# Performance work log

Measured on AMD Instinct MI355X. Metric: run time of the kernel, lower is better.

## Reference

```python
import jax, jax.numpy as jnp
import numpy as np

M, K, N, GROUP = 64, 4096, 11008, 128
NGROUPS = K // GROUP  # 32


def setup_inputs() -> dict:
    key = jax.random.key(0)
    k1, k2, k3, k4, k5 = jax.random.split(key, 5)
    x = jax.random.normal(k1, (M, K), dtype=jnp.float32)
    # packed int4 weights: 8 nibbles per int32, full 32-bit entropy
    qweight = jax.random.bits(k2, (K // 8, N), dtype=jnp.uint32).astype(jnp.int32)
    qzeros = jax.random.bits(k3, (NGROUPS, N // 8), dtype=jnp.uint32).astype(jnp.int32)
    scales = jax.random.uniform(k4, (NGROUPS, N), dtype=jnp.float32, minval=0.001, maxval=0.02)
    bias = jax.random.normal(k5, (N,), dtype=jnp.float32) * 0.01
    return {"x": x, "qweight": qweight, "qzeros": qzeros, "scales": scales, "bias": bias}


def dequantize(qweight, qzeros, scales):
    shifts = jnp.arange(8, dtype=jnp.int32) * 4  # nibble bit offsets 0..28
    # unpack weights: [K//8, N] -> [K//8, 8, N] -> [NGROUPS, GROUP, N]
    w = (jnp.right_shift(qweight[:, None, :], shifts[None, :, None]) & 15)
    w = w.reshape(-1, GROUP, qweight.shape[1])
    # unpack zeros: [NGROUPS, N//8] -> [NGROUPS, N//8, 8] -> [NGROUPS, 1, N]; GPTQ stores zero-1
    z = (jnp.right_shift(qzeros[:, :, None], shifts[None, None, :]) & 15) + 1
    z = z.reshape(z.shape[0], 1, -1)
    # scale * (q - zero), per group: [NGROUPS, GROUP, N] -> [K, N]
    W = scales[:, None, :] * (w - z).astype(scales.dtype)
    return W.reshape(-1, W.shape[2])


def reference(x, qweight, qzeros, scales, bias):
    W = dequantize(qweight, qzeros, scales)  # [K, N] fp32
    return jnp.matmul(x, W.astype(x.dtype)) + bias
```

## Files before the change

kernel.cpp:

```cpp
#include <hip/hip_runtime.h>
#include <hip/hip_bf16.h>

namespace {

constexpr int MM = 64;
constexpr int KK = 4096;
constexpr int NN = 11008;
constexpr int NZROW = NN / 8;
constexpr int BN = 128;
constexpr int KSPLIT = 8;
constexpr int KSEG = KK / KSPLIT;
constexpr int NTILES = NN / BN;
constexpr int BK = 32;
constexpr int NCH = KSEG / BK;
constexpr int NG = 4;
constexpr size_t XB_OFF_BYTES = (size_t)KSPLIT * MM * NN * 4;
constexpr size_t WS_NEED = XB_OFF_BYTES + (size_t)MM * KK * 2;

typedef float f32x4 __attribute__((ext_vector_type(4)));
typedef short s16x8 __attribute__((ext_vector_type(8)));
typedef int   i32x4 __attribute__((ext_vector_type(4)));

__device__ __forceinline__ int pack_bf16(float a, float b) {
  union { __hip_bfloat162 h; int i; } u;
  u.h.x = __float2bfloat16(a);
  u.h.y = __float2bfloat16(b);
  return u.i;
}

__global__ __launch_bounds__(256) void xcvt_kernel(
    const float* __restrict__ x, unsigned short* __restrict__ xb)
{
  const int i8 = (blockIdx.x * 256 + threadIdx.x) * 8;
  const f32x4 a = *(const f32x4*)(x + i8);
  const f32x4 b = *(const f32x4*)(x + i8 + 4);
  i32x4 p;
  p.x = pack_bf16(a.x, a.y);
  p.y = pack_bf16(a.z, a.w);
  p.z = pack_bf16(b.x, b.y);
  p.w = pack_bf16(b.z, b.w);
  *(i32x4*)(xb + i8) = p;
}

__global__ __launch_bounds__(256) void prep_kernel(
    const float* __restrict__ bias, float* __restrict__ out)
{
  const int i = blockIdx.x * 256 + threadIdx.x;
  out[i] = bias[i % NN];
}

__global__ __launch_bounds__(256) void reduce_kernel(
    const float* __restrict__ ws, const float* __restrict__ bias,
    float* __restrict__ out)
{
  const int i4 = (blockIdx.x * 256 + threadIdx.x) * 4;
  f32x4 acc = *(const f32x4*)(bias + (i4 % NN));
  #pragma unroll
  for (int s = 0; s < KSPLIT; ++s)
    acc += *(const f32x4*)(ws + (size_t)s * (MM * NN) + i4);
  *(f32x4*)(out + i4) = acc;
}

template<bool WS>
__global__ __launch_bounds__(256, 4) void gptq_gemm_kernel(
    const float* __restrict__ x, const int* __restrict__ qw,
    const int* __restrict__ qz, const float* __restrict__ scales,
    const unsigned short* __restrict__ xb, float* __restrict__ out)
{
  const int tid  = threadIdx.x;
  const int wave = tid >> 6;
  const int lane = tid & 63;
  const int c    = lane & 15;
  const int quad = lane >> 4;

  const int ks     = blockIdx.x & 7;
  const int ntile  = blockIdx.x >> 3;
  const int n0     = ntile * BN;
  const int kbase0 = ks * KSEG;
  const int grp0   = kbase0 >> 7;

  const int ncol = n0 + wave * 32 + c;

  const unsigned short* xbb = xb + (size_t)c * KK + kbase0 + quad * 8;
  const int* qwb = qw + ((size_t)(kbase0 >> 3) + quad) * NN + ncol;

  f32x4 acc[8];
  #pragma unroll
  for (int t = 0; t < 8; ++t) acc[t] = {0.f, 0.f, 0.f, 0.f};

  s16x8 pA[2][4];
  int   pB0[4], pB1[4];
  float pS0[2], pS1[2];
  int   pZ0[2], pZ1[2];
  float s0, s1, C0, C1;

  auto ldA = [&](int i) {
    const unsigned short* xp = xbb + i * BK;
    #pragma unroll
    for (int r = 0; r < 4; ++r)
      pA[i & 1][r] = *(const s16x8*)(xp + (size_t)r * 16 * KK);
  };
  auto pfB = [&](int i) {
    const int* qp = qwb + (size_t)i * 4 * NN;
    pB0[i & 3] = qp[0];
    pB1[i & 3] = qp[16];
  };
  auto pfS = [&](int g) {
    const int sl = g & 1;
    const float* sp = scales + (size_t)(grp0 + g) * NN + ncol;
    pS0[sl] = sp[0];
    pS1[sl] = sp[16];
    const int* zp = qz + (size_t)(grp0 + g) * NZROW + (ncol >> 3);
    pZ0[sl] = zp[0];
    pZ1[sl] = zp[2];
  };
  auto setSC = [&](int g) {
    const int sl = g & 1;
    const int sh = (ncol & 7) * 4;
    s0 = pS0[sl];
    s1 = pS1[sl];
    C0 = __int_as_float(0x4B000000 + ((pZ0[sl] >> sh) & 15) + 1);
    C1 = __int_as_float(0x4B000000 + ((pZ1[sl] >> sh) & 15) + 1);
  };
  auto dq8 = [&](int v, float s, float C) -> i32x4 {
    i32x4 p;
    p.x = pack_bf16(s * (__int_as_float(((v      ) & 15) | 0x4B000000) - C),
                    s * (__int_as_float(((v >>  4) & 15) | 0x4B000000) - C));
    p.y = pack_bf16(s * (__int_as_float(((v >>  8) & 15) | 0x4B000000) - C),
                    s * (__int_as_float(((v >> 12) & 15) | 0x4B000000) - C));
    p.z = pack_bf16(s * (__int_as_float(((v >> 16) & 15) | 0x4B000000) - C),
                    s * (__int_as_float(((v >> 20) & 15) | 0x4B000000) - C));
    p.w = pack_bf16(s * (__int_as_float(((v >> 24) & 15) | 0x4B000000) - C),
                    s * (__int_as_float(((v >> 28) & 15) | 0x4B000000) - C));
    return p;
  };
  auto ldA_f32 = [&](int i, int r) -> s16x8 {
    const float* xa = x + (size_t)(r * 16 + c) * KK + kbase0 + i * BK + quad * 8;
    const f32x4 a0 = *(const f32x4*)xa;
    const f32x4 a1 = *(const f32x4*)(xa + 4);
    union { i32x4 i4; s16x8 s8; } ua;
    ua.i4.x = pack_bf16(a0.x, a0.y);
    ua.i4.y = pack_bf16(a0.z, a0.w);
    ua.i4.z = pack_bf16(a1.x, a1.y);
    ua.i4.w = pack_bf16(a1.z, a1.w);
    return ua.s8;
  };

  pfS(0);
  pfB(0); pfB(1); pfB(2);
  if (WS) ldA(0);
  setSC(0);
  pfS(1);

  #pragma unroll
  for (int i = 0; i < NCH; ++i) {
    if (i + 3 < NCH) pfB(i + 3);
    if (WS && i + 1 < NCH) ldA(i + 1);

    union { i32x4 i4; s16x8 s8; } u0, u1;
    u0.i4 = dq8(pB0[i & 3], s0, C0);
    u1.i4 = dq8(pB1[i & 3], s1, C1);

    #pragma unroll
    for (int r = 0; r < 4; ++r) {
      const s16x8 af = WS ? pA[i & 1][r] : ldA_f32(i, r);
      acc[r * 2 + 0] = __builtin_amdgcn_mfma_f32_16x16x32_bf16(af, u0.s8, acc[r * 2 + 0], 0, 0, 0);
      acc[r * 2 + 1] = __builtin_amdgcn_mfma_f32_16x16x32_bf16(af, u1.s8, acc[r * 2 + 1], 0, 0, 0);
    }

    if ((i & 3) == 3) {
      const int g = i >> 2;
      if (g + 1 < NG) { setSC(g + 1); if (g + 2 < NG) pfS(g + 2); }
    }
  }

  if (WS) {
    float* wsp = out + (size_t)ks * (MM * NN);
    #pragma unroll
    for (int r = 0; r < 4; ++r) {
      #pragma unroll
      for (int t = 0; t < 2; ++t) {
        const f32x4 a = acc[r * 2 + t];
        float* op = wsp + (size_t)(r * 16 + quad * 4) * NN + ncol + t * 16;
        op[0]      = a.x;
        op[NN]     = a.y;
        op[2 * NN] = a.z;
        op[3 * NN] = a.w;
      }
    }
  } else {
    #pragma unroll
    for (int r = 0; r < 4; ++r) {
      #pragma unroll
      for (int t = 0; t < 2; ++t) {
        const f32x4 a = acc[r * 2 + t];
        float* op = out + (size_t)(r * 16 + quad * 4) * NN + ncol + t * 16;
        atomicAdd(&op[0],          a.x);
        atomicAdd(&op[NN],         a.y);
        atomicAdd(&op[2 * NN],     a.z);
        atomicAdd(&op[3 * NN],     a.w);
      }
    }
  }
}

}

extern "C" void kernel_launch(void* const* d_in, const int* in_sizes, int n_in,
                              void* d_out, int out_size, void* d_ws, size_t ws_size,
                              hipStream_t stream) {
  const float* x      = (const float*)d_in[0];
  const int*   qw     = (const int*)d_in[1];
  const int*   qz     = (const int*)d_in[2];
  const float* scales = (const float*)d_in[3];
  const float* bias   = (const float*)d_in[4];
  float* out = (float*)d_out;

  if (ws_size >= WS_NEED) {
    float* ws = (float*)d_ws;
    unsigned short* xb = (unsigned short*)((char*)d_ws + XB_OFF_BYTES);
    xcvt_kernel<<<(MM * KK) / 2048, 256, 0, stream>>>(x, xb);
    gptq_gemm_kernel<true><<<NTILES * KSPLIT, 256, 0, stream>>>(x, qw, qz, scales, xb, ws);
    reduce_kernel<<<(MM * NN) / 1024, 256, 0, stream>>>(ws, bias, out);
  } else {
    prep_kernel<<<(MM * NN) / 256, 256, 0, stream>>>(bias, out);
    gptq_gemm_kernel<false><<<NTILES * KSPLIT, 256, 0, stream>>>(x, qw, qz, scales, nullptr, out);
  }
}
```

Measured before the change: 108.5 us.

## Fuse split-K reduction into single kernel via in-block LDS wave reduction

Replaces the three-kernel pipeline (x bf16 conversion, split-K GEMM writing partials to a workspace, reduction kernel) with one kernel. Each block covers 32 columns and its four waves each handle a quarter of K; the partials are reduced through LDS, bias is added, and the result is stored directly. This removes the large fp32 workspace write/read traffic and two extra launches. In exchange x is read as fp32 and converted inside the GEMM, with no software prefetch of A, and the grid shrinks to 344 blocks, which may lower occupancy on a 256-CU part.

```diff
diff --git a/kernel.cpp b/kernel.cpp
--- a/kernel.cpp
+++ b/kernel.cpp
@@ -7,15 +7,14 @@
 constexpr int KK = 4096;
 constexpr int NN = 11008;
 constexpr int NZROW = NN / 8;
-constexpr int BN = 128;
-constexpr int KSPLIT = 8;
-constexpr int KSEG = KK / KSPLIT;
-constexpr int NTILES = NN / BN;
+constexpr int WB = 32;
+constexpr int NWAVE = 4;
+constexpr int KSEG = KK / NWAVE;
 constexpr int BK = 32;
 constexpr int NCH = KSEG / BK;
-constexpr int NG = 4;
-constexpr size_t XB_OFF_BYTES = (size_t)KSPLIT * MM * NN * 4;
-constexpr size_t WS_NEED = XB_OFF_BYTES + (size_t)MM * KK * 2;
+constexpr int NG = KSEG / 128;
+constexpr int NBLK = NN / WB;
+constexpr int RST = 33;
 
 typedef float f32x4 __attribute__((ext_vector_type(4)));
 typedef short s16x8 __attribute__((ext_vector_type(8)));
@@ -28,78 +27,37 @@
   return u.i;
 }
 
-__global__ __launch_bounds__(256) void xcvt_kernel(
-    const float* __restrict__ x, unsigned short* __restrict__ xb)
-{
-  const int i8 = (blockIdx.x * 256 + threadIdx.x) * 8;
-  const f32x4 a = *(const f32x4*)(x + i8);
-  const f32x4 b = *(const f32x4*)(x + i8 + 4);
-  i32x4 p;
-  p.x = pack_bf16(a.x, a.y);
-  p.y = pack_bf16(a.z, a.w);
-  p.z = pack_bf16(b.x, b.y);
-  p.w = pack_bf16(b.z, b.w);
-  *(i32x4*)(xb + i8) = p;
-}
-
-__global__ __launch_bounds__(256) void prep_kernel(
-    const float* __restrict__ bias, float* __restrict__ out)
-{
-  const int i = blockIdx.x * 256 + threadIdx.x;
-  out[i] = bias[i % NN];
-}
-
-__global__ __launch_bounds__(256) void reduce_kernel(
-    const float* __restrict__ ws, const float* __restrict__ bias,
-    float* __restrict__ out)
-{
-  const int i4 = (blockIdx.x * 256 + threadIdx.x) * 4;
-  f32x4 acc = *(const f32x4*)(bias + (i4 % NN));
-  #pragma unroll
-  for (int s = 0; s < KSPLIT; ++s)
-    acc += *(const f32x4*)(ws + (size_t)s * (MM * NN) + i4);
-  *(f32x4*)(out + i4) = acc;
-}
-
-template<bool WS>
 __global__ __launch_bounds__(256, 4) void gptq_gemm_kernel(
     const float* __restrict__ x, const int* __restrict__ qw,
     const int* __restrict__ qz, const float* __restrict__ scales,
-    const unsigned short* __restrict__ xb, float* __restrict__ out)
+    const float* __restrict__ bias, float* __restrict__ out)
 {
+  __shared__ float red[NWAVE * MM * RST];
+
   const int tid  = threadIdx.x;
   const int wave = tid >> 6;
   const int lane = tid & 63;
   const int c    = lane & 15;
   const int quad = lane >> 4;
 
-  const int ks     = blockIdx.x & 7;
-  const int ntile  = blockIdx.x >> 3;
-  const int n0     = ntile * BN;
-  const int kbase0 = ks * KSEG;
+  const int n0     = blockIdx.x * WB;
+  const int kbase0 = wave * KSEG;
   const int grp0   = kbase0 >> 7;
 
-  const int ncol = n0 + wave * 32 + c;
+  const int ncol = n0 + c;
 
-  const unsigned short* xbb = xb + (size_t)c * KK + kbase0 + quad * 8;
   const int* qwb = qw + ((size_t)(kbase0 >> 3) + quad) * NN + ncol;
+  const float* xab = x + (size_t)c * KK + kbase0 + quad * 8;
 
   f32x4 acc[8];
   #pragma unroll
   for (int t = 0; t < 8; ++t) acc[t] = {0.f, 0.f, 0.f, 0.f};
 
-  s16x8 pA[2][4];
   int   pB0[4], pB1[4];
   float pS0[2], pS1[2];
   int   pZ0[2], pZ1[2];
   float s0, s1, C0, C1;
 
-  auto ldA = [&](int i) {
-    const unsigned short* xp = xbb + i * BK;
-    #pragma unroll
-    for (int r = 0; r < 4; ++r)
-      pA[i & 1][r] = *(const s16x8*)(xp + (size_t)r * 16 * KK);
-  };
   auto pfB = [&](int i) {
     const int* qp = qwb + (size_t)i * 4 * NN;
     pB0[i & 3] = qp[0];
@@ -134,8 +92,8 @@
                     s * (__int_as_float(((v >> 28) & 15) | 0x4B000000) - C));
     return p;
   };
-  auto ldA_f32 = [&](int i, int r) -> s16x8 {
-    const float* xa = x + (size_t)(r * 16 + c) * KK + kbase0 + i * BK + quad * 8;
+  auto ldA = [&](int i, int r) -> s16x8 {
+    const float* xa = xab + (size_t)r * 16 * KK + i * BK;
     const f32x4 a0 = *(const f32x4*)xa;
     const f32x4 a1 = *(const f32x4*)(xa + 4);
     union { i32x4 i4; s16x8 s8; } ua;
@@ -148,14 +106,12 @@
 
   pfS(0);
   pfB(0); pfB(1); pfB(2);
-  if (WS) ldA(0);
   setSC(0);
   pfS(1);
 
   #pragma unroll
   for (int i = 0; i < NCH; ++i) {
     if (i + 3 < NCH) pfB(i + 3);
-    if (WS && i + 1 < NCH) ldA(i + 1);
 
     union { i32x4 i4; s16x8 s8; } u0, u1;
     u0.i4 = dq8(pB0[i & 3], s0, C0);
@@ -163,7 +119,7 @@
 
     #pragma unroll
     for (int r = 0; r < 4; ++r) {
-      const s16x8 af = WS ? pA[i & 1][r] : ldA_f32(i, r);
+      const s16x8 af = ldA(i, r);
       acc[r * 2 + 0] = __builtin_amdgcn_mfma_f32_16x16x32_bf16(af, u0.s8, acc[r * 2 + 0], 0, 0, 0);
       acc[r * 2 + 1] = __builtin_amdgcn_mfma_f32_16x16x32_bf16(af, u1.s8, acc[r * 2 + 1], 0, 0, 0);
     }
@@ -174,34 +130,37 @@
     }
   }
 
-  if (WS) {
-    float* wsp = out + (size_t)ks * (MM * NN);
+  float* rw = red + (size_t)(wave * MM) * RST;
+  #pragma unroll
+  for (int r = 0; r < 4; ++r) {
     #pragma unroll
-    for (int r = 0; r < 4; ++r) {
-      #pragma unroll
-      for (int t = 0; t < 2; ++t) {
-        const f32x4 a = acc[r * 2 + t];
-        float* op = wsp + (size_t)(r * 16 + quad * 4) * NN + ncol + t * 16;
-        op[0]      = a.x;
-        op[NN]     = a.y;
-        op[2 * NN] = a.z;
-        op[3 * NN] = a.w;
-      }
-    }
-  } else {
-    #pragma unroll
-    for (int r = 0; r < 4; ++r) {
-      #pragma unroll
-      for (int t = 0; t < 2; ++t) {
-        const f32x4 a = acc[r * 2 + t];
-        float* op = out + (size_t)(r * 16 + quad * 4) * NN + ncol + t * 16;
-        atomicAdd(&op[0],          a.x);
-        atomicAdd(&op[NN],         a.y);
-        atomicAdd(&op[2 * NN],     a.z);
-        atomicAdd(&op[3 * NN],     a.w);
-      }
+    for (int t = 0; t < 2; ++t) {
+      const f32x4 a = acc[r * 2 + t];
+      float* p = rw + (r * 16 + quad * 4) * RST + c + t * 16;
+      p[0]       = a.x;
+      p[RST]     = a.y;
+      p[2 * RST] = a.z;
+      p[3 * RST] = a.w;
     }
   }
+  __syncthreads();
+
+  const int row  = tid >> 2;
+  const int col0 = (tid & 3) * 8;
+  const f32x4 b0 = *(const f32x4*)(bias + n0 + col0);
+  const f32x4 b1 = *(const f32x4*)(bias + n0 + col0 + 4);
+  float sum[8] = {b0.x, b0.y, b0.z, b0.w, b1.x, b1.y, b1.z, b1.w};
+  #pragma unroll
+  for (int w = 0; w < NWAVE; ++w) {
+    const float* rp = red + (size_t)(w * MM + row) * RST + col0;
+    #pragma unroll
+    for (int j = 0; j < 8; ++j) sum[j] += rp[j];
+  }
+  float* op = out + (size_t)row * NN + n0 + col0;
+  f32x4 o0 = {sum[0], sum[1], sum[2], sum[3]};
+  f32x4 o1 = {sum[4], sum[5], sum[6], sum[7]};
+  *(f32x4*)op       = o0;
+  *(f32x4*)(op + 4) = o1;
 }
 
 }
@@ -215,15 +174,7 @@
   const float* scales = (const float*)d_in[3];
   const float* bias   = (const float*)d_in[4];
   float* out = (float*)d_out;
+  (void)d_ws; (void)ws_size;
 
-  if (ws_size >= WS_NEED) {
-    float* ws = (float*)d_ws;
-    unsigned short* xb = (unsigned short*)((char*)d_ws + XB_OFF_BYTES);
-    xcvt_kernel<<<(MM * KK) / 2048, 256, 0, stream>>>(x, xb);
-    gptq_gemm_kernel<true><<<NTILES * KSPLIT, 256, 0, stream>>>(x, qw, qz, scales, xb, ws);
-    reduce_kernel<<<(MM * NN) / 1024, 256, 0, stream>>>(ws, bias, out);
-  } else {
-    prep_kernel<<<(MM * NN) / 256, 256, 0, stream>>>(bias, out);
-    gptq_gemm_kernel<false><<<NTILES * KSPLIT, 256, 0, stream>>>(x, qw, qz, scales, nullptr, out);
-  }
+  gptq_gemm_kernel<<<NBLK, 256, 0, stream>>>(x, qw, qz, scales, bias, out);
 }
```

After: 132.4 us. +22.0%, slower.

## Drop bf16 pre-conversion kernel and halve per-wave column tile

Applied to the files above, without the earlier changes.

Removes the separate x-to-bf16 conversion kernel and converts fp32 activations to bf16 inside the GEMM loop. Each wave now covers 16 columns instead of 32, so the block tile shrinks from 128 to 64 columns, doubling the grid and raising the occupancy hint to 5. This saves a kernel launch and the extra workspace traffic, but each block reloads fp32 x (twice the bytes) with less reuse per load, and x is now read without a prefetch pipeline.

```diff
diff --git a/kernel.cpp b/kernel.cpp
--- a/kernel.cpp
+++ b/kernel.cpp
@@ -7,15 +7,15 @@
 constexpr int KK = 4096;
 constexpr int NN = 11008;
 constexpr int NZROW = NN / 8;
-constexpr int BN = 128;
+constexpr int WCOL = 16;
+constexpr int BCOL = 64;
 constexpr int KSPLIT = 8;
 constexpr int KSEG = KK / KSPLIT;
-constexpr int NTILES = NN / BN;
 constexpr int BK = 32;
 constexpr int NCH = KSEG / BK;
-constexpr int NG = 4;
-constexpr size_t XB_OFF_BYTES = (size_t)KSPLIT * MM * NN * 4;
-constexpr size_t WS_NEED = XB_OFF_BYTES + (size_t)MM * KK * 2;
+constexpr int NG = KSEG / 128;
+constexpr int NT = NN / BCOL;
+constexpr size_t WS_NEED = (size_t)KSPLIT * MM * NN * 4;
 
 typedef float f32x4 __attribute__((ext_vector_type(4)));
 typedef short s16x8 __attribute__((ext_vector_type(8)));
@@ -26,20 +26,6 @@
   u.h.x = __float2bfloat16(a);
   u.h.y = __float2bfloat16(b);
   return u.i;
-}
-
-__global__ __launch_bounds__(256) void xcvt_kernel(
-    const float* __restrict__ x, unsigned short* __restrict__ xb)
-{
-  const int i8 = (blockIdx.x * 256 + threadIdx.x) * 8;
-  const f32x4 a = *(const f32x4*)(x + i8);
-  const f32x4 b = *(const f32x4*)(x + i8 + 4);
-  i32x4 p;
-  p.x = pack_bf16(a.x, a.y);
-  p.y = pack_bf16(a.z, a.w);
-  p.z = pack_bf16(b.x, b.y);
-  p.w = pack_bf16(b.z, b.w);
-  *(i32x4*)(xb + i8) = p;
 }
 
 __global__ __launch_bounds__(256) void prep_kernel(
@@ -61,11 +47,11 @@
   *(f32x4*)(out + i4) = acc;
 }
 
-template<bool WS>
-__global__ __launch_bounds__(256, 4) void gptq_gemm_kernel(
+template<bool ATOMIC>
+__global__ __launch_bounds__(256, 5) void gptq_gemm_kernel(
     const float* __restrict__ x, const int* __restrict__ qw,
     const int* __restrict__ qz, const float* __restrict__ scales,
-    const unsigned short* __restrict__ xb, float* __restrict__ out)
+    float* __restrict__ out)
 {
   const int tid  = threadIdx.x;
   const int wave = tid >> 6;
@@ -74,98 +60,77 @@
   const int quad = lane >> 4;
 
   const int ks     = blockIdx.x & 7;
-  const int ntile  = blockIdx.x >> 3;
-  const int n0     = ntile * BN;
+  const int nt     = blockIdx.x >> 3;
+  const int n0     = nt * BCOL;
   const int kbase0 = ks * KSEG;
   const int grp0   = kbase0 >> 7;
 
-  const int ncol = n0 + wave * 32 + c;
+  const int ncol = n0 + wave * WCOL + c;
 
-  const unsigned short* xbb = xb + (size_t)c * KK + kbase0 + quad * 8;
   const int* qwb = qw + ((size_t)(kbase0 >> 3) + quad) * NN + ncol;
+  const float* xab = x + (size_t)c * KK + kbase0 + quad * 8;
 
-  f32x4 acc[8];
+  f32x4 acc[4];
   #pragma unroll
-  for (int t = 0; t < 8; ++t) acc[t] = {0.f, 0.f, 0.f, 0.f};
+  for (int r = 0; r < 4; ++r) acc[r] = {0.f, 0.f, 0.f, 0.f};
 
-  s16x8 pA[2][4];
-  int   pB0[4], pB1[4];
-  float pS0[2], pS1[2];
-  int   pZ0[2], pZ1[2];
-  float s0, s1, C0, C1;
+  int   pB[4];
+  float pS[2];
+  int   pZ[2];
+  float s0, C0;
 
-  auto ldA = [&](int i) {
-    const unsigned short* xp = xbb + i * BK;
-    #pragma unroll
-    for (int r = 0; r < 4; ++r)
-      pA[i & 1][r] = *(const s16x8*)(xp + (size_t)r * 16 * KK);
-  };
-  auto pfB = [&](int i) {
-    const int* qp = qwb + (size_t)i * 4 * NN;
-    pB0[i & 3] = qp[0];
-    pB1[i & 3] = qp[16];
-  };
+  auto pfB = [&](int i) { pB[i & 3] = qwb[(size_t)i * 4 * NN]; };
   auto pfS = [&](int g) {
     const int sl = g & 1;
-    const float* sp = scales + (size_t)(grp0 + g) * NN + ncol;
-    pS0[sl] = sp[0];
-    pS1[sl] = sp[16];
-    const int* zp = qz + (size_t)(grp0 + g) * NZROW + (ncol >> 3);
-    pZ0[sl] = zp[0];
-    pZ1[sl] = zp[2];
+    pS[sl] = scales[(size_t)(grp0 + g) * NN + ncol];
+    pZ[sl] = qz[(size_t)(grp0 + g) * NZROW + (ncol >> 3)];
   };
   auto setSC = [&](int g) {
     const int sl = g & 1;
     const int sh = (ncol & 7) * 4;
-    s0 = pS0[sl];
-    s1 = pS1[sl];
-    C0 = __int_as_float(0x4B000000 + ((pZ0[sl] >> sh) & 15) + 1);
-    C1 = __int_as_float(0x4B000000 + ((pZ1[sl] >> sh) & 15) + 1);
+    s0 = pS[sl];
+    C0 = __int_as_float(0x4B000000 + ((pZ[sl] >> sh) & 15) + 1);
   };
-  auto dq8 = [&](int v, float s, float C) -> i32x4 {
+  auto dq8 = [&](int v) -> i32x4 {
     i32x4 p;
-    p.x = pack_bf16(s * (__int_as_float(((v      ) & 15) | 0x4B000000) - C),
-                    s * (__int_as_float(((v >>  4) & 15) | 0x4B000000) - C));
-    p.y = pack_bf16(s * (__int_as_float(((v >>  8) & 15) | 0x4B000000) - C),
-                    s * (__int_as_float(((v >> 12) & 15) | 0x4B000000) - C));
-    p.z = pack_bf16(s * (__int_as_float(((v >> 16) & 15) | 0x4B000000) - C),
-                    s * (__int_as_float(((v >> 20) & 15) | 0x4B000000) - C));
-    p.w = pack_bf16(s * (__int_as_float(((v >> 24) & 15) | 0x4B000000) - C),
-                    s * (__int_as_float(((v >> 28) & 15) | 0x4B000000) - C));
+    p.x = pack_bf16(s0 * (__int_as_float(((v      ) & 15) | 0x4B000000) - C0),
+                    s0 * (__int_as_float(((v >>  4) & 15) | 0x4B000000) - C0));
+    p.y = pack_bf16(s0 * (__int_as_float(((v >>  8) & 15) | 0x4B000000) - C0),
+                    s0 * (__int_as_float(((v >> 12) & 15) | 0x4B000000) - C0));
+    p.z = pack_bf16(s0 * (__int_as_float(((v >> 16) & 15) | 0x4B000000) - C0),
+                    s0 * (__int_as_float(((v >> 20) & 15) | 0x4B000000) - C0));
+    p.w = pack_bf16(s0 * (__int_as_float(((v >> 24) & 15) | 0x4B000000) - C0),
+                    s0 * (__int_as_float(((v >> 28) & 15) | 0x4B000000) - C0));
     return p;
-  };
-  auto ldA_f32 = [&](int i, int r) -> s16x8 {
-    const float* xa = x + (size_t)(r * 16 + c) * KK + kbase0 + i * BK + quad * 8;
-    const f32x4 a0 = *(const f32x4*)xa;
-    const f32x4 a1 = *(const f32x4*)(xa + 4);
-    union { i32x4 i4; s16x8 s8; } ua;
-    ua.i4.x = pack_bf16(a0.x, a0.y);
-    ua.i4.y = pack_bf16(a0.z, a0.w);
-    ua.i4.z = pack_bf16(a1.x, a1.y);
-    ua.i4.w = pack_bf16(a1.z, a1.w);
-    return ua.s8;
   };
 
   pfS(0);
   pfB(0); pfB(1); pfB(2);
-  if (WS) ldA(0);
   setSC(0);
   pfS(1);
 
   #pragma unroll
   for (int i = 0; i < NCH; ++i) {
+    f32x4 a0[4], a1[4];
+    #pragma unroll
+    for (int r = 0; r < 4; ++r) {
+      const float* xa = xab + (size_t)r * 16 * KK + i * BK;
+      a0[r] = *(const f32x4*)xa;
+      a1[r] = *(const f32x4*)(xa + 4);
+    }
     if (i + 3 < NCH) pfB(i + 3);
-    if (WS && i + 1 < NCH) ldA(i + 1);
 
-    union { i32x4 i4; s16x8 s8; } u0, u1;
-    u0.i4 = dq8(pB0[i & 3], s0, C0);
-    u1.i4 = dq8(pB1[i & 3], s1, C1);
+    union { i32x4 i4; s16x8 s8; } ub;
+    ub.i4 = dq8(pB[i & 3]);
 
     #pragma unroll
     for (int r = 0; r < 4; ++r) {
-      const s16x8 af = WS ? pA[i & 1][r] : ldA_f32(i, r);
-      acc[r * 2 + 0] = __builtin_amdgcn_mfma_f32_16x16x32_bf16(af, u0.s8, acc[r * 2 + 0], 0, 0, 0);
-      acc[r * 2 + 1] = __builtin_amdgcn_mfma_f32_16x16x32_bf16(af, u1.s8, acc[r * 2 + 1], 0, 0, 0);
+      union { i32x4 i4; s16x8 s8; } ua;
+      ua.i4.x = pack_bf16(a0[r].x, a0[r].y);
+      ua.i4.y = pack_bf16(a0[r].z, a0[r].w);
+      ua.i4.z = pack_bf16(a1[r].x, a1[r].y);
+      ua.i4.w = pack_bf16(a1[r].z, a1[r].w);
+      acc[r] = __builtin_amdgcn_mfma_f32_16x16x32_bf16(ua.s8, ub.s8, acc[r], 0, 0, 0);
     }
 
     if ((i & 3) == 3) {
@@ -174,32 +139,26 @@
     }
   }
 
-  if (WS) {
+  if (ATOMIC) {
+    #pragma unroll
+    for (int r = 0; r < 4; ++r) {
+      const f32x4 a = acc[r];
+      float* op = out + (size_t)(r * 16 + quad * 4) * NN + ncol;
+      atomicAdd(&op[0],      a.x);
+      atomicAdd(&op[NN],     a.y);
+      atomicAdd(&op[2 * NN], a.z);
+      atomicAdd(&op[3 * NN], a.w);
+    }
+  } else {
     float* wsp = out + (size_t)ks * (MM * NN);
     #pragma unroll
     for (int r = 0; r < 4; ++r) {
-      #pragma unroll
-      for (int t = 0; t < 2; ++t) {
-        const f32x4 a = acc[r * 2 + t];
-        float* op = wsp + (size_t)(r * 16 + quad * 4) * NN + ncol + t * 16;
-        op[0]      = a.x;
-        op[NN]     = a.y;
-        op[2 * NN] = a.z;
-        op[3 * NN] = a.w;
-      }
-    }
-  } else {
-    #pragma unroll
-    for (int r = 0; r < 4; ++r) {
-      #pragma unroll
-      for (int t = 0; t < 2; ++t) {
-        const f32x4 a = acc[r * 2 + t];
-        float* op = out + (size_t)(r * 16 + quad * 4) * NN + ncol + t * 16;
-        atomicAdd(&op[0],          a.x);
-        atomicAdd(&op[NN],         a.y);
-        atomicAdd(&op[2 * NN],     a.z);
-        atomicAdd(&op[3 * NN],     a.w);
-      }
+      const f32x4 a = acc[r];
+      float* op = wsp + (size_t)(r * 16 + quad * 4) * NN + ncol;
+      op[0]      = a.x;
+      op[NN]     = a.y;
+      op[2 * NN] = a.z;
+      op[3 * NN] = a.w;
     }
   }
 }
@@ -218,12 +177,10 @@
 
   if (ws_size >= WS_NEED) {
     float* ws = (float*)d_ws;
-    unsigned short* xb = (unsigned short*)((char*)d_ws + XB_OFF_BYTES);
-    xcvt_kernel<<<(MM * KK) / 2048, 256, 0, stream>>>(x, xb);
-    gptq_gemm_kernel<true><<<NTILES * KSPLIT, 256, 0, stream>>>(x, qw, qz, scales, xb, ws);
+    gptq_gemm_kernel<false><<<NT * KSPLIT, 256, 0, stream>>>(x, qw, qz, scales, ws);
     reduce_kernel<<<(MM * NN) / 1024, 256, 0, stream>>>(ws, bias, out);
   } else {
     prep_kernel<<<(MM * NN) / 256, 256, 0, stream>>>(bias, out);
-    gptq_gemm_kernel<false><<<NTILES * KSPLIT, 256, 0, stream>>>(x, qw, qz, scales, nullptr, out);
+    gptq_gemm_kernel<true><<<NT * KSPLIT, 256, 0, stream>>>(x, qw, qz, scales, out);
   }
 }
```

After: 166.9 us. 1.54x slower.
